# Kernel tuning notes

Hardware: AMD Instinct MI355X
Metric: run time of the kernel (lower is better)

Reference implementation:

```python
import jax, jax.numpy as jnp
import numpy as np

B, S, SC, E, H = 2, 2048, 2048, 1024, 16
D = E // H
EPS = 1e-6


def _layernorm(x, g, b):
    m = jnp.mean(x, axis=-1, keepdims=True)
    v = jnp.mean((x - m) ** 2, axis=-1, keepdims=True)
    return (x - m) / jnp.sqrt(v + EPS) * g + b


def _mha(xk, xv, xq, Wk, Wv, Wq, Wo, bo, masked):
    # per-head projections, vectorized over the head axis: [B,Sx,E] x [H,E,D] -> [B,H,Sx,D]
    K = jnp.einsum('bse,hed->bhsd', xk, Wk)
    V = jnp.einsum('bse,hed->bhsd', xv, Wv)
    Q = jnp.einsum('bqe,hed->bhqd', xq, Wq)
    scores = jnp.einsum('bhqd,bhkd->bhqk', Q, K)  # [B,H,Sq,Sk]
    sk = xk.shape[1]
    if masked:
        causal = jnp.triu(jnp.ones((xq.shape[1], sk), dtype=bool), k=1)
        scores = jnp.where(causal, -jnp.inf, scores)
    att = jax.nn.softmax(scores / jnp.sqrt(jnp.asarray(sk, scores.dtype)), axis=-1)
    out = jnp.einsum('bhqk,bhkd->bhqd', att, V)
    out = out.transpose(0, 2, 1, 3).reshape(out.shape[0], out.shape[2], -1)  # concat heads -> [B,Sq,E]
    return jax.nn.relu(out @ Wo + bo)  # Dense(emb_sz, relu) output projection


def setup_inputs():
    key = jax.random.key(0)
    ks = jax.random.split(key, 16)
    w = lambda k, shape: jax.random.normal(k, shape, jnp.float32) * 0.02
    return {
        'inputs': jax.random.normal(ks[0], (B, S, E), jnp.float32),
        'context_seq': jax.random.normal(ks[1], (B, SC, E), jnp.float32),
        'Wk1': w(ks[2], (H, E, D)), 'Wv1': w(ks[3], (H, E, D)), 'Wq1': w(ks[4], (H, E, D)),
        'Wo1': w(ks[5], (E, E)), 'bo1': jnp.zeros((E,), jnp.float32),
        'Wk2': w(ks[6], (H, E, D)), 'Wv2': w(ks[7], (H, E, D)), 'Wq2': w(ks[8], (H, E, D)),
        'Wo2': w(ks[9], (E, E)), 'bo2': jnp.zeros((E,), jnp.float32),
        'Wf': w(ks[10], (E, E)), 'bf': jnp.zeros((E,), jnp.float32),
        'g1': jnp.ones((E,), jnp.float32), 'b1': jnp.zeros((E,), jnp.float32),
        'g2': jnp.ones((E,), jnp.float32), 'b2': jnp.zeros((E,), jnp.float32),
        'g3': jnp.ones((E,), jnp.float32), 'b3': jnp.zeros((E,), jnp.float32),
    }


def reference(inputs, context_seq, Wk1, Wv1, Wq1, Wo1, bo1,
              Wk2, Wv2, Wq2, Wo2, bo2, Wf, bf,
              g1, b1, g2, b2, g3, b3):
    # masked multi-head self-attention + residual + LN1 (dropout is identity at inference)
    a = _mha(inputs, inputs, inputs, Wk1, Wv1, Wq1, Wo1, bo1, masked=True)
    a = _layernorm(inputs + a, g1, b1)
    # unmasked cross-attention: K/V from context, Q from previous output
    c = _mha(context_seq, context_seq, a, Wk2, Wv2, Wq2, Wo2, bo2, masked=False)
    c = _layernorm(c + c, g2, b2)  # faithful to source: residual adds output to itself
    # FFN (single Dense(emb_sz, relu)) + residual + LN3
    f = jax.nn.relu(c @ Wf + bf)
    return _layernorm(c + f, g3, b3)
```

## Files before the change

### kernel.cpp

```cpp
#include <hip/hip_runtime.h>
#include <stdint.h>
#include <stddef.h>

typedef __bf16 bf16;
typedef __bf16 bf16x8 __attribute__((ext_vector_type(8)));
typedef __bf16 bf16x4 __attribute__((ext_vector_type(4)));
typedef float  f32x4  __attribute__((ext_vector_type(4)));
typedef uint32_t u32x4 __attribute__((ext_vector_type(4)));

#define MFMA(a, b, c) __builtin_amdgcn_mfma_f32_16x16x32_bf16((a), (b), (c), 0, 0, 0)
#define SWZE(row, chunk) (((row) << 6) + ((((chunk) ^ ((row) & 7))) << 3))

static __device__ __forceinline__ void gload_lds16(const void* g, void* l) {
  __builtin_amdgcn_global_load_lds((const __attribute__((address_space(1))) void*)g,
                                   (__attribute__((address_space(3))) void*)l,
                                   16, 0, 0);
}
static __device__ __forceinline__ void waitvm0() {
  asm volatile("s_waitcnt vmcnt(0)" ::: "memory");
}
static __device__ __forceinline__ float expq(float x) {
  float r;
  asm("v_exp_f32 %0, %1" : "=v"(r) : "v"(x));
  return r;
}
static __device__ __forceinline__ float rcpq(float x) {
  float r;
  asm("v_rcp_f32 %0, %1" : "=v"(r) : "v"(x));
  return r;
}
static __device__ __forceinline__ uint32_t cvtpk_bf16(float lo, float hi) {
  uint32_t r;
  asm("v_cvt_pk_bf16_f32 %0, %1, %2" : "=v"(r) : "v"(lo), "v"(hi));
  return r;
}
static __device__ __forceinline__ int xcd_swz(int orig, int nwg) {
  return (orig & 7) * (nwg >> 3) + (orig >> 3);
}
static __device__ __forceinline__ int vperm_store(int s) {
  return (s & ~31) | (((s >> 3) & 1) << 4) | (((s >> 2) & 1) << 3) |
         (((s >> 4) & 1) << 2) | (s & 3);
}

__global__ __launch_bounds__(256) void prep_k(
    const float* __restrict__ inp, const float* __restrict__ ctx,
    bf16* __restrict__ XB, bf16* __restrict__ CB,
    const float* __restrict__ Wq1, const float* __restrict__ Wk1,
    const float* __restrict__ Wv1, const float* __restrict__ Wq2,
    const float* __restrict__ Wk2, const float* __restrict__ Wv2,
    bf16* __restrict__ WQKV1, bf16* __restrict__ WQ2, bf16* __restrict__ WKV2,
    const float* __restrict__ Wo1, const float* __restrict__ Wo2,
    const float* __restrict__ Wf,
    bf16* __restrict__ WO1, bf16* __restrict__ WO2, bf16* __restrict__ WFt) {
  const int tid = threadIdx.x;
  int bx = blockIdx.x;
  if (bx < 8192) {
    const float* s = bx < 4096 ? inp : ctx;
    bf16* d = bx < 4096 ? XB : CB;
    size_t idx = (size_t)(bx & 4095) * 256 + tid;
    float4 v = *(const float4*)(s + idx * 4);
    bf16x4 o;
    o[0] = (bf16)v.x; o[1] = (bf16)v.y; o[2] = (bf16)v.z; o[3] = (bf16)v.w;
    *(bf16x4*)(d + idx * 4) = o;
    return;
  }
  bx -= 8192;
  __shared__ float T[64][65];
  if (bx < 1536) {
    const int wi = bx >> 8, sub = bx & 255;
    const float* src = (wi == 0) ? Wq1 : (wi == 1) ? Wk1 : (wi == 2) ? Wv1
                     : (wi == 3) ? Wq2 : (wi == 4) ? Wk2 : Wv2;
    bf16* dst = (wi == 0) ? WQKV1 : (wi == 1) ? WQKV1 + 1048576
              : (wi == 2) ? WQKV1 + 2097152 : (wi == 3) ? WQ2
              : (wi == 4) ? WKV2 : WKV2 + 1048576;
    const int e0 = (sub & 15) * 64, h = sub >> 4;
    const int er = tid >> 4, dof = (tid & 15) * 4;
#pragma unroll
    for (int i = 0; i < 4; ++i) {
      int e = i * 16 + er;
      float4 v = *(const float4*)(src + ((size_t)h * 1024 + e0 + e) * 64 + dof);
      T[e][dof] = v.x; T[e][dof + 1] = v.y; T[e][dof + 2] = v.z; T[e][dof + 3] = v.w;
    }
    __syncthreads();
    const int dr = tid >> 3, eo = (tid & 7) * 8;
#pragma unroll
    for (int i = 0; i < 2; ++i) {
      int d = i * 32 + dr;
      bf16x8 ov;
#pragma unroll
      for (int j = 0; j < 8; ++j) ov[j] = (bf16)T[eo + j][d];
      *(bf16x8*)(dst + ((size_t)h * 64 + d) * 1024 + e0 + eo) = ov;
    }
    return;
  }
  bx -= 1536;
  {
    const int wi = bx >> 8, sub = bx & 255;
    const float* src = (wi == 0) ? Wo1 : (wi == 1) ? Wo2 : Wf;
    bf16* dst = (wi == 0) ? WO1 : (wi == 1) ? WO2 : WFt;
    const int k0 = (sub & 15) * 64, n0 = (sub >> 4) * 64;
    const int kr = tid >> 4, no = (tid & 15) * 4;
#pragma unroll
    for (int i = 0; i < 4; ++i) {
      int k = i * 16 + kr;
      float4 v = *(const float4*)(src + (size_t)(k0 + k) * 1024 + n0 + no);
      T[k][no] = v.x; T[k][no + 1] = v.y; T[k][no + 2] = v.z; T[k][no + 3] = v.w;
    }
    __syncthreads();
    const int nr = tid >> 3, ko = (tid & 7) * 8;
#pragma unroll
    for (int i = 0; i < 2; ++i) {
      int n = i * 32 + nr;
      bf16x8 ov;
#pragma unroll
      for (int j = 0; j < 8; ++j) ov[j] = (bf16)T[ko + j][n];
      *(bf16x8*)(dst + (size_t)(n0 + n) * 1024 + k0 + ko) = ov;
    }
  }
}

template <int EPI>
static __device__ __forceinline__ void gemm_body(
    const bf16* __restrict__ A, const bf16* __restrict__ Bt,
    bf16* __restrict__ Cb, float* __restrict__ Cf,
    const float* __restrict__ bias, const float* __restrict__ resid,
    int N, int K, float mul, int m0, int n0, bf16* As, bf16* Bs,
    bf16* __restrict__ Vt, int colV) {
  const int tid = threadIdx.x;
  const int l = tid & 63, w = tid >> 6;
  const int l15 = l & 15, g4 = l >> 4;
  const int wr = w >> 1, wc = w & 1;
  f32x4 acc[4][4] = {};
  const int crow = tid >> 3, sj = tid & 7;
  for (int k0 = 0; k0 < K; k0 += 64) {
#pragma unroll
    for (int i = 0; i < 4; ++i) {
      int row = i * 32 + crow;
      int je = ((sj ^ (row & 7)) << 3);
      gload_lds16(A + (size_t)(m0 + row) * K + (k0 + je), (char*)As + (i * 256 + tid) * 16);
      gload_lds16(Bt + (size_t)(n0 + row) * K + (k0 + je), (char*)Bs + (i * 256 + tid) * 16);
    }
    __syncthreads();
#pragma unroll
    for (int kk = 0; kk < 2; ++kk) {
      bf16x8 af[4], bfr[4];
#pragma unroll
      for (int x = 0; x < 4; ++x) {
        af[x]  = *(const bf16x8*)&As[SWZE(wr * 64 + x * 16 + l15, kk * 4 + g4)];
        bfr[x] = *(const bf16x8*)&Bs[SWZE(wc * 64 + x * 16 + l15, kk * 4 + g4)];
      }
      __builtin_amdgcn_s_setprio(1);
#pragma unroll
      for (int mf = 0; mf < 4; ++mf)
#pragma unroll
        for (int nf = 0; nf < 4; ++nf)
          acc[mf][nf] = MFMA(af[mf], bfr[nf], acc[mf][nf]);
      __builtin_amdgcn_s_setprio(0);
    }
    __syncthreads();
  }
  if (EPI == 2 && n0 >= colV) {
#pragma unroll
    for (int mf = 0; mf < 4; ++mf)
#pragma unroll
      for (int nf = 0; nf < 4; ++nf) {
        int colrel = n0 + wc * 64 + nf * 16 + l15 - colV;
        int h = colrel >> 6, d = colrel & 63;
        int row = m0 + wr * 64 + mf * 16 + g4 * 4;
        int b = row >> 11, s = row & 2047;
        bf16x4 pv;
#pragma unroll
        for (int r = 0; r < 4; ++r) pv[r] = (bf16)acc[mf][nf][r];
        *(bf16x4*)(Vt + (((size_t)(b * 16 + h) * 64 + d) * 2048 + vperm_store(s))) = pv;
      }
    return;
  }
#pragma unroll
  for (int mf = 0; mf < 4; ++mf)
#pragma unroll
    for (int nf = 0; nf < 4; ++nf)
#pragma unroll
      for (int r = 0; r < 4; ++r) {
        int row = m0 + wr * 64 + mf * 16 + g4 * 4 + r;
        int col = n0 + wc * 64 + nf * 16 + l15;
        size_t idx = (size_t)row * N + col;
        float v = acc[mf][nf][r];
        if (EPI == 1) {
          v = mul * fmaxf(v + bias[col], 0.f);
          if (resid) v += resid[idx];
          Cf[idx] = v;
        } else {
          Cb[idx] = (bf16)v;
        }
      }
}

__global__ __launch_bounds__(256) void gemm_qkv_k(
    const bf16* __restrict__ A, const bf16* __restrict__ Bt,
    bf16* __restrict__ Cb, bf16* __restrict__ Vt, int N, int K, int colV) {
  __shared__ __align__(16) bf16 As[128 * 64];
  __shared__ __align__(16) bf16 Bs[128 * 64];
  int swz = xcd_swz(blockIdx.y * gridDim.x + blockIdx.x, gridDim.x * gridDim.y);
  int bx = swz % gridDim.x, by = swz / gridDim.x;
  gemm_body<2>(A, Bt, Cb, nullptr, nullptr, nullptr, N, K, 1.f,
               by * 128, bx * 128, As, Bs, Vt, colV);
}

__global__ __launch_bounds__(256) void gemm_bt2_k(
    const bf16* __restrict__ A0, const bf16* __restrict__ Bt0, bf16* __restrict__ C0,
    const bf16* __restrict__ A1, const bf16* __restrict__ Bt1, bf16* __restrict__ C1,
    bf16* __restrict__ Vt, int K) {
  __shared__ __align__(16) bf16 As[128 * 64];
  __shared__ __align__(16) bf16 Bs[128 * 64];
  int swz = xcd_swz(blockIdx.y * gridDim.x + blockIdx.x, gridDim.x * gridDim.y);
  int bx = swz % gridDim.x, by = swz / gridDim.x;
  if (bx < 8)
    gemm_body<0>(A0, Bt0, C0, nullptr, nullptr, nullptr, 1024, K, 1.f,
                 by * 128, bx * 128, As, Bs, nullptr, 1 << 30);
  else
    gemm_body<2>(A1, Bt1, C1, nullptr, nullptr, nullptr, 2048, K, 1.f,
                 by * 128, (bx - 8) * 128, As, Bs, Vt, 1024);
}

template <int EPI>
__global__ __launch_bounds__(512) void gemm64_k(
    const bf16* __restrict__ A, const bf16* __restrict__ Bt,
    bf16* __restrict__ Cb, float* __restrict__ Cf,
    const float* __restrict__ bias, const float* __restrict__ resid,
    int N, int K, float mul) {
  __shared__ __align__(16) bf16 As[64 * 64];
  __shared__ __align__(16) bf16 Bs[128 * 64];
  const int tid = threadIdx.x;
  const int l = tid & 63, w = tid >> 6;
  const int l15 = l & 15, g4 = l >> 4;
  const int wr = w >> 2, wc = w & 3;
  int swz = xcd_swz(blockIdx.y * gridDim.x + blockIdx.x, gridDim.x * gridDim.y);
  const int m0 = (swz / gridDim.x) * 64, n0 = (swz % gridDim.x) * 128;
  f32x4 acc[2][2] = {};
  const int crow = tid >> 3, sj = tid & 7;
  const int jeA = ((sj ^ (crow & 7)) << 3);
  for (int k0 = 0; k0 < K; k0 += 64) {
    gload_lds16(A + (size_t)(m0 + crow) * K + (k0 + jeA), (char*)As + tid * 16);
#pragma unroll
    for (int i = 0; i < 2; ++i) {
      int row = i * 64 + crow;
      int je = ((sj ^ (row & 7)) << 3);
      gload_lds16(Bt + (size_t)(n0 + row) * K + (k0 + je), (char*)Bs + (i * 512 + tid) * 16);
    }
    __syncthreads();
#pragma unroll
    for (int kk = 0; kk < 2; ++kk) {
      bf16x8 af[2], bfr[2];
#pragma unroll
      for (int x = 0; x < 2; ++x) {
        af[x]  = *(const bf16x8*)&As[SWZE(wr * 32 + x * 16 + l15, kk * 4 + g4)];
        bfr[x] = *(const bf16x8*)&Bs[SWZE(wc * 32 + x * 16 + l15, kk * 4 + g4)];
      }
      __builtin_amdgcn_s_setprio(1);
#pragma unroll
      for (int mf = 0; mf < 2; ++mf)
#pragma unroll
        for (int nf = 0; nf < 2; ++nf)
          acc[mf][nf] = MFMA(af[mf], bfr[nf], acc[mf][nf]);
      __builtin_amdgcn_s_setprio(0);
    }
    __syncthreads();
  }
#pragma unroll
  for (int mf = 0; mf < 2; ++mf)
#pragma unroll
    for (int nf = 0; nf < 2; ++nf)
#pragma unroll
      for (int r = 0; r < 4; ++r) {
        int row = m0 + wr * 32 + mf * 16 + g4 * 4 + r;
        int col = n0 + wc * 32 + nf * 16 + l15;
        size_t idx = (size_t)row * N + col;
        float v = acc[mf][nf][r];
        if (EPI == 0) {
          Cb[idx] = (bf16)v;
        } else {
          v = mul * fmaxf(v + bias[col], 0.f);
          if (resid) v += resid[idx];
          Cf[idx] = v;
        }
      }
}

template <int CAUSAL>
__global__ __launch_bounds__(512) void attn_k(
    const bf16* __restrict__ Q, int ldq, size_t sBq,
    const bf16* __restrict__ Kp, int ldk, size_t sBk,
    const bf16* __restrict__ Vt,
    bf16* __restrict__ O, int ldo, size_t sBo,
    int Sk) {
  __shared__ __align__(16) char smem[32768];
  bf16* const KsBase = (bf16*)smem;
  bf16* const VsBase = (bf16*)(smem + 16384);
  const int tid = threadIdx.x;
  const int l = tid & 63, w = tid >> 6;
  const int l15 = l & 15, g4 = l >> 4;
  const int qh = w >> 1, kh = w & 1;
  const int orig = blockIdx.y * gridDim.x + blockIdx.x;
  int qt, bh;
  if (CAUSAL) {
    const int slot = orig >> 8, s = orig & 255;
    const int pb = s & 15;
    qt = slot ? (15 - pb) : pb;
    bh = (s >> 4) * 2 + slot;
  } else {
    const int swz = xcd_swz(orig, gridDim.x * gridDim.y);
    qt = swz % gridDim.x;
    bh = swz / gridDim.x;
  }
  const int b = bh >> 4, h = bh & 15;
  const int nT = Sk >> 6;
  const int total = CAUSAL ? (2 * qt + 2) : nT;
  const int q0b = qt * 128;
  const int qw = q0b + qh * 32;
  const bf16* Qb = Q + (size_t)b * sBq + h * 64;
  const bf16* Kb = Kp + (size_t)b * sBk + h * 64;
  const bf16* Vb = Vt + ((size_t)bh * 64) * Sk;
  bf16* Ob = O + (size_t)b * sBo + h * 64;
  const float sc2 = rsqrtf((float)Sk) * 1.442695040888963f;

  bf16x8 qf[2][2];
#pragma unroll
  for (int qg = 0; qg < 2; ++qg)
#pragma unroll
    for (int kk = 0; kk < 2; ++kk) {
      bf16x8 t8 = *(const bf16x8*)(Qb + (size_t)(qw + qg * 16 + l15) * ldq + kk * 32 + g4 * 8);
#pragma unroll
      for (int j = 0; j < 8; ++j) t8[j] = (bf16)((float)t8[j] * sc2);
      qf[qg][kk] = t8;
    }

  bf16x8 onesb;
#pragma unroll
  for (int j = 0; j < 8; ++j) onesb[j] = (bf16)1.0f;

  f32x4 o[2][4] = {};
  f32x4 ol[2] = {};

  const int srow = tid >> 3, sj = tid & 7;
  const int je = ((sj ^ (srow & 7)) << 3);
  auto stage = [&](int ch, int bufi) {
    gload_lds16(Kb + (size_t)(ch * 64 + srow) * ldk + je,
                (char*)(KsBase + bufi * 4096) + tid * 16);
    gload_lds16(Vb + (size_t)srow * Sk + ch * 64 + je,
                (char*)(VsBase + bufi * 4096) + tid * 16);
  };

  stage(0, 0);
  waitvm0();
  __builtin_amdgcn_s_barrier();

  int cur = 0;

  for (int i = 0; i < total; ++i) {
    if (i + 1 < total) stage(i + 1, cur ^ 1);

    const int k0 = i * 64;
    const bf16* ks = KsBase + cur * 4096;
    const bf16* vs = VsBase + cur * 4096;

    f32x4 s[2][2] = {};
    __builtin_amdgcn_s_setprio(1);
#pragma unroll
    for (int ksub = 0; ksub < 2; ++ksub)
#pragma unroll
      for (int kk = 0; kk < 2; ++kk) {
        bf16x8 kf = *(const bf16x8*)&ks[SWZE(kh * 32 + ksub * 16 + l15, kk * 4 + g4)];
        s[ksub][0] = MFMA(kf, qf[0][kk], s[ksub][0]);
        s[ksub][1] = MFMA(kf, qf[1][kk], s[ksub][1]);
      }
    __builtin_amdgcn_s_setprio(0);

    if (CAUSAL && i >= total - 2) {
#pragma unroll
      for (int ksub = 0; ksub < 2; ++ksub)
#pragma unroll
        for (int qg = 0; qg < 2; ++qg)
#pragma unroll
          for (int r = 0; r < 4; ++r)
            if ((k0 + kh * 32 + ksub * 16 + g4 * 4 + r) > (qw + qg * 16 + l15))
              s[ksub][qg][r] = -3e38f;
    }

#pragma unroll
    for (int ksub = 0; ksub < 2; ++ksub)
#pragma unroll
      for (int qg = 0; qg < 2; ++qg) {
        s[ksub][qg][0] = expq(s[ksub][qg][0]);
        s[ksub][qg][1] = expq(s[ksub][qg][1]);
        s[ksub][qg][2] = expq(s[ksub][qg][2]);
        s[ksub][qg][3] = expq(s[ksub][qg][3]);
      }

    bf16x8 vf[4];
#pragma unroll
    for (int nf2 = 0; nf2 < 4; ++nf2)
      vf[nf2] = *(const bf16x8*)&vs[SWZE(nf2 * 16 + l15, kh * 4 + g4)];

    __builtin_amdgcn_s_setprio(1);
#pragma unroll
    for (int qg = 0; qg < 2; ++qg) {
      u32x4 td;
      td[0] = cvtpk_bf16(s[0][qg][0], s[0][qg][1]);
      td[1] = cvtpk_bf16(s[0][qg][2], s[0][qg][3]);
      td[2] = cvtpk_bf16(s[1][qg][0], s[1][qg][1]);
      td[3] = cvtpk_bf16(s[1][qg][2], s[1][qg][3]);
      bf16x8 pa = __builtin_bit_cast(bf16x8, td);
#pragma unroll
      for (int nf2 = 0; nf2 < 4; ++nf2)
        o[qg][nf2] = MFMA(pa, vf[nf2], o[qg][nf2]);
      ol[qg] = MFMA(pa, onesb, ol[qg]);
    }
    __builtin_amdgcn_s_setprio(0);

    waitvm0();
    __builtin_amdgcn_s_barrier();
    cur ^= 1;
  }

  {
    float* sc = (float*)smem;
    float* my = sc + (size_t)(qh * 64 + l) * 21;
#pragma unroll
    for (int qg = 0; qg < 2; ++qg) {
      __syncthreads();
      if (kh == 1) {
#pragma unroll
        for (int nf2 = 0; nf2 < 4; ++nf2)
#pragma unroll
          for (int r = 0; r < 4; ++r) my[nf2 * 4 + r] = o[qg][nf2][r];
#pragma unroll
        for (int r = 0; r < 4; ++r) my[16 + r] = ol[qg][r];
      }
      __syncthreads();
      if (kh == 0) {
        float inv[4];
#pragma unroll
        for (int r = 0; r < 4; ++r) inv[r] = rcpq(ol[qg][r] + my[16 + r]);
#pragma unroll
        for (int nf2 = 0; nf2 < 4; ++nf2)
#pragma unroll
          for (int r = 0; r < 4; ++r) {
            float v = (o[qg][nf2][r] + my[nf2 * 4 + r]) * inv[r];
            Ob[(size_t)(qw + qg * 16 + g4 * 4 + r) * ldo + nf2 * 16 + l15] = (bf16)v;
          }
      }
    }
  }
}

__global__ __launch_bounds__(256) void ln_k(const float* __restrict__ X,
                                            const float* __restrict__ g,
                                            const float* __restrict__ bta,
                                            bf16* __restrict__ outb,
                                            float* __restrict__ outf) {
  const int tid = threadIdx.x;
  const size_t row = blockIdx.x;
  const float* x = X + row * 1024;
  float4 v = *(const float4*)(x + tid * 4);
  float sum = v.x + v.y + v.z + v.w;
  float sq = v.x * v.x + v.y * v.y + v.z * v.z + v.w * v.w;
#pragma unroll
  for (int m = 1; m < 64; m <<= 1) {
    sum += __shfl_xor(sum, m);
    sq += __shfl_xor(sq, m);
  }
  __shared__ float s1[4], s2[4];
  int w = tid >> 6;
  if ((tid & 63) == 0) { s1[w] = sum; s2[w] = sq; }
  __syncthreads();
  sum = s1[0] + s1[1] + s1[2] + s1[3];
  sq = s2[0] + s2[1] + s2[2] + s2[3];
  float mean = sum * (1.f / 1024.f);
  float var = sq * (1.f / 1024.f) - mean * mean;
  float inv = rsqrtf(var + 1e-6f);
  float4 gv = *(const float4*)(g + tid * 4);
  float4 bv = *(const float4*)(bta + tid * 4);
  float y0 = (v.x - mean) * inv * gv.x + bv.x;
  float y1 = (v.y - mean) * inv * gv.y + bv.y;
  float y2 = (v.z - mean) * inv * gv.z + bv.z;
  float y3 = (v.w - mean) * inv * gv.w + bv.w;
  if (outb) {
    bf16x4 ob;
    ob[0] = (bf16)y0; ob[1] = (bf16)y1; ob[2] = (bf16)y2; ob[3] = (bf16)y3;
    *(bf16x4*)(outb + row * 1024 + tid * 4) = ob;
  }
  if (outf) {
    float4 of;
    of.x = y0; of.y = y1; of.z = y2; of.w = y3;
    *(float4*)(outf + row * 1024 + tid * 4) = of;
  }
}

extern "C" void kernel_launch(void* const* d_in, const int* in_sizes, int n_in,
                              void* d_out, int out_size, void* d_ws, size_t ws_size,
                              hipStream_t stream) {
  (void)in_sizes; (void)n_in; (void)out_size; (void)ws_size;
  const float* inp = (const float*)d_in[0];
  const float* ctx = (const float*)d_in[1];
  const float* Wk1 = (const float*)d_in[2];
  const float* Wv1 = (const float*)d_in[3];
  const float* Wq1 = (const float*)d_in[4];
  const float* Wo1 = (const float*)d_in[5];
  const float* bo1 = (const float*)d_in[6];
  const float* Wk2 = (const float*)d_in[7];
  const float* Wv2 = (const float*)d_in[8];
  const float* Wq2 = (const float*)d_in[9];
  const float* Wo2 = (const float*)d_in[10];
  const float* bo2 = (const float*)d_in[11];
  const float* Wf = (const float*)d_in[12];
  const float* bfp = (const float*)d_in[13];
  const float* g1 = (const float*)d_in[14];
  const float* b1 = (const float*)d_in[15];
  const float* g2 = (const float*)d_in[16];
  const float* b2 = (const float*)d_in[17];
  const float* g3 = (const float*)d_in[18];
  const float* b3 = (const float*)d_in[19];
  float* out = (float*)d_out;

  char* ws = (char*)d_ws;
  size_t off = 0;
  auto alloc = [&](size_t bytes) {
    char* p = ws + off;
    off += (bytes + 255) & ~(size_t)255;
    return p;
  };
  bf16* XB = (bf16*)alloc(4096ULL * 1024 * 2);
  bf16* CB = (bf16*)alloc(4096ULL * 1024 * 2);
  bf16* WQKV1 = (bf16*)alloc(3072ULL * 1024 * 2);
  bf16* WO1 = (bf16*)alloc(1024ULL * 1024 * 2);
  bf16* WQ2 = (bf16*)alloc(1024ULL * 1024 * 2);
  bf16* WKV2 = (bf16*)alloc(2048ULL * 1024 * 2);
  bf16* WO2 = (bf16*)alloc(1024ULL * 1024 * 2);
  bf16* WFt = (bf16*)alloc(1024ULL * 1024 * 2);
  bf16* QKV1 = (bf16*)alloc(4096ULL * 3072 * 2);
  bf16* V1T = (bf16*)alloc(32ULL * 64 * 2048 * 2);
  bf16* ATT1 = (bf16*)alloc(4096ULL * 1024 * 2);
  float* T1 = (float*)alloc(4096ULL * 1024 * 4);
  float* CF = (float*)alloc(4096ULL * 1024 * 4);

  bf16* AB = XB;
  bf16* CBf = CB;
  bf16* Q2 = QKV1;
  bf16* KV2 = QKV1 + 4096ULL * 1024;
  bf16* V2T = V1T;
  bf16* ATT2 = ATT1;
  float* T2 = T1;
  float* T3 = T1;

  dim3 b256(256);
  dim3 b512(512);

  prep_k<<<10496, b256, 0, stream>>>(inp, ctx, XB, CB,
                                     Wq1, Wk1, Wv1, Wq2, Wk2, Wv2,
                                     WQKV1, WQ2, WKV2,
                                     Wo1, Wo2, Wf, WO1, WO2, WFt);

  gemm_qkv_k<<<dim3(24, 32), b256, 0, stream>>>(XB, WQKV1, QKV1, V1T, 3072, 1024, 2048);
  attn_k<1><<<dim3(16, 32), b512, 0, stream>>>(QKV1, 3072, (size_t)2048 * 3072,
                                               QKV1 + 1024, 3072, (size_t)2048 * 3072,
                                               V1T, ATT1, 1024, (size_t)2048 * 1024, 2048);
  gemm64_k<1><<<dim3(8, 64), b512, 0, stream>>>(ATT1, WO1, nullptr, T1, bo1, inp,
                                                1024, 1024, 1.f);
  ln_k<<<4096, b256, 0, stream>>>(T1, g1, b1, AB, nullptr);

  gemm_bt2_k<<<dim3(24, 32), b256, 0, stream>>>(AB, WQ2, Q2, CB, WKV2, KV2, V2T, 1024);
  attn_k<0><<<dim3(16, 32), b512, 0, stream>>>(Q2, 1024, (size_t)2048 * 1024,
                                               KV2, 2048, (size_t)2048 * 2048,
                                               V2T, ATT2, 1024, (size_t)2048 * 1024, 2048);
  gemm64_k<1><<<dim3(8, 64), b512, 0, stream>>>(ATT2, WO2, nullptr, T2, bo2, nullptr,
                                                1024, 1024, 2.f);
  ln_k<<<4096, b256, 0, stream>>>(T2, g2, b2, CBf, CF);

  gemm64_k<1><<<dim3(8, 64), b512, 0, stream>>>(CBf, WFt, nullptr, T3, bfp, CF,
                                                1024, 1024, 1.f);
  ln_k<<<4096, b256, 0, stream>>>(T3, g3, b3, nullptr, out);
}
```

Baseline: 218.3 us.

## Split causal attention KV range across two blocks and add combine kernel

The causal self-attention kernel now splits each query tile's key range into two halves, each handled by a separate block, doubling the grid to 1024 blocks. Each block writes unnormalized partial outputs (bf16) and row sums to scratch buffers, and a new combine kernel adds the halves and normalizes into the attention output. This replaces the previous load-balancing pairing of short and long query tiles with an even split of work per block. It adds a second launch and extra global traffic for the partials, and it rounds the partial sums to bf16 before combining.

```diff
diff --git a/kernel.cpp b/kernel.cpp
--- a/kernel.cpp
+++ b/kernel.cpp
@@ -286,13 +286,13 @@
       }
 }
 
-template <int CAUSAL>
+template <int MODE>
 __global__ __launch_bounds__(512) void attn_k(
     const bf16* __restrict__ Q, int ldq, size_t sBq,
     const bf16* __restrict__ Kp, int ldk, size_t sBk,
     const bf16* __restrict__ Vt,
     bf16* __restrict__ O, int ldo, size_t sBo,
-    int Sk) {
+    int Sk, bf16* __restrict__ Opart, float* __restrict__ Lpart) {
   __shared__ __align__(16) char smem[32768];
   bf16* const KsBase = (bf16*)smem;
   bf16* const VsBase = (bf16*)(smem + 16384);
@@ -301,12 +301,10 @@
   const int l15 = l & 15, g4 = l >> 4;
   const int qh = w >> 1, kh = w & 1;
   const int orig = blockIdx.y * gridDim.x + blockIdx.x;
-  int qt, bh;
-  if (CAUSAL) {
-    const int slot = orig >> 8, s = orig & 255;
-    const int pb = s & 15;
-    qt = slot ? (15 - pb) : pb;
-    bh = (s >> 4) * 2 + slot;
+  int qt, bh, half = 0, rest = 0;
+  if (MODE == 1) {
+    half = orig >> 9; rest = orig & 511;
+    bh = rest >> 4; qt = rest & 15;
   } else {
     const int swz = xcd_swz(orig, gridDim.x * gridDim.y);
     qt = swz % gridDim.x;
@@ -314,7 +312,8 @@
   }
   const int b = bh >> 4, h = bh & 15;
   const int nT = Sk >> 6;
-  const int total = CAUSAL ? (2 * qt + 2) : nT;
+  const int nCh = (MODE == 1) ? (qt + 1) : nT;
+  const int chStart = (MODE == 1) ? half * (qt + 1) : 0;
   const int q0b = qt * 128;
   const int qw = q0b + qh * 32;
   const bf16* Qb = Q + (size_t)b * sBq + h * 64;
@@ -350,16 +349,17 @@
                 (char*)(VsBase + bufi * 4096) + tid * 16);
   };
 
-  stage(0, 0);
+  stage(chStart, 0);
   waitvm0();
   __builtin_amdgcn_s_barrier();
 
   int cur = 0;
 
-  for (int i = 0; i < total; ++i) {
-    if (i + 1 < total) stage(i + 1, cur ^ 1);
-
-    const int k0 = i * 64;
+  for (int i = 0; i < nCh; ++i) {
+    if (i + 1 < nCh) stage(chStart + i + 1, cur ^ 1);
+
+    const int gch = chStart + i;
+    const int k0 = gch * 64;
     const bf16* ks = KsBase + cur * 4096;
     const bf16* vs = VsBase + cur * 4096;
 
@@ -375,7 +375,8 @@
       }
     __builtin_amdgcn_s_setprio(0);
 
-    if (CAUSAL && i >= total - 2) {
+    bool needMask = (MODE == 1) ? (gch >= 2 * qt) : false;
+    if (needMask) {
 #pragma unroll
       for (int ksub = 0; ksub < 2; ++ksub)
 #pragma unroll
@@ -438,18 +439,59 @@
       }
       __syncthreads();
       if (kh == 0) {
-        float inv[4];
-#pragma unroll
-        for (int r = 0; r < 4; ++r) inv[r] = rcpq(ol[qg][r] + my[16 + r]);
-#pragma unroll
-        for (int nf2 = 0; nf2 < 4; ++nf2)
-#pragma unroll
-          for (int r = 0; r < 4; ++r) {
-            float v = (o[qg][nf2][r] + my[nf2 * 4 + r]) * inv[r];
-            Ob[(size_t)(qw + qg * 16 + g4 * 4 + r) * ldo + nf2 * 16 + l15] = (bf16)v;
+        if (MODE == 1) {
+          bf16* op = Opart + (size_t)orig * 8192;
+          float* lp = Lpart + (size_t)orig * 128;
+#pragma unroll
+          for (int nf2 = 0; nf2 < 4; ++nf2)
+#pragma unroll
+            for (int r = 0; r < 4; ++r) {
+              float v = o[qg][nf2][r] + my[nf2 * 4 + r];
+              op[(qh * 32 + qg * 16 + g4 * 4 + r) * 64 + nf2 * 16 + l15] = (bf16)v;
+            }
+          if (l15 == 0) {
+#pragma unroll
+            for (int r = 0; r < 4; ++r)
+              lp[qh * 32 + qg * 16 + g4 * 4 + r] = ol[qg][r] + my[16 + r];
           }
-      }
-    }
+        } else {
+          float inv[4];
+#pragma unroll
+          for (int r = 0; r < 4; ++r) inv[r] = rcpq(ol[qg][r] + my[16 + r]);
+#pragma unroll
+          for (int nf2 = 0; nf2 < 4; ++nf2)
+#pragma unroll
+            for (int r = 0; r < 4; ++r) {
+              float v = (o[qg][nf2][r] + my[nf2 * 4 + r]) * inv[r];
+              Ob[(size_t)(qw + qg * 16 + g4 * 4 + r) * ldo + nf2 * 16 + l15] = (bf16)v;
+            }
+        }
+      }
+    }
+  }
+}
+
+__global__ __launch_bounds__(256) void combine_k(
+    const bf16* __restrict__ Opart, const float* __restrict__ Lpart,
+    bf16* __restrict__ ATT) {
+  const int c = blockIdx.x;
+  const int qt = c & 15, bh = c >> 4, b = bh >> 4, h = bh & 15;
+  const bf16* o0 = Opart + (size_t)c * 8192;
+  const bf16* o1 = Opart + (size_t)(512 + c) * 8192;
+  const float* l0 = Lpart + (size_t)c * 128;
+  const float* l1 = Lpart + (size_t)(512 + c) * 128;
+  const int t = threadIdx.x;
+#pragma unroll
+  for (int e = 0; e < 8; ++e) {
+    int idx = e * 1024 + t * 4;
+    int q = idx >> 6, d = idx & 63;
+    float inv = rcpq(l0[q] + l1[q]);
+    bf16x4 a = *(const bf16x4*)(o0 + idx);
+    bf16x4 bb = *(const bf16x4*)(o1 + idx);
+    bf16x4 r;
+#pragma unroll
+    for (int j = 0; j < 4; ++j) r[j] = (bf16)(((float)a[j] + (float)bb[j]) * inv);
+    *(bf16x4*)(ATT + ((size_t)(b * 2048 + qt * 128 + q) * 1024) + h * 64 + d) = r;
   }
 }
 
@@ -542,6 +584,8 @@
   bf16* ATT1 = (bf16*)alloc(4096ULL * 1024 * 2);
   float* T1 = (float*)alloc(4096ULL * 1024 * 4);
   float* CF = (float*)alloc(4096ULL * 1024 * 4);
+  bf16* OPart = (bf16*)alloc(1024ULL * 8192 * 2);
+  float* LPart = (float*)alloc(1024ULL * 128 * 4);
 
   bf16* AB = XB;
   bf16* CBf = CB;
@@ -561,9 +605,11 @@
                                      Wo1, Wo2, Wf, WO1, WO2, WFt);
 
   gemm_qkv_k<<<dim3(24, 32), b256, 0, stream>>>(XB, WQKV1, QKV1, V1T, 3072, 1024, 2048);
-  attn_k<1><<<dim3(16, 32), b512, 0, stream>>>(QKV1, 3072, (size_t)2048 * 3072,
+  attn_k<1><<<dim3(32, 32), b512, 0, stream>>>(QKV1, 3072, (size_t)2048 * 3072,
                                                QKV1 + 1024, 3072, (size_t)2048 * 3072,
-                                               V1T, ATT1, 1024, (size_t)2048 * 1024, 2048);
+                                               V1T, ATT1, 1024, (size_t)2048 * 1024, 2048,
+                                               OPart, LPart);
+  combine_k<<<512, b256, 0, stream>>>(OPart, LPart, ATT1);
   gemm64_k<1><<<dim3(8, 64), b512, 0, stream>>>(ATT1, WO1, nullptr, T1, bo1, inp,
                                                 1024, 1024, 1.f);
   ln_k<<<4096, b256, 0, stream>>>(T1, g1, b1, AB, nullptr);
@@ -571,7 +617,8 @@
   gemm_bt2_k<<<dim3(24, 32), b256, 0, stream>>>(AB, WQ2, Q2, CB, WKV2, KV2, V2T, 1024);
   attn_k<0><<<dim3(16, 32), b512, 0, stream>>>(Q2, 1024, (size_t)2048 * 1024,
                                                KV2, 2048, (size_t)2048 * 2048,
-                                               V2T, ATT2, 1024, (size_t)2048 * 1024, 2048);
+                                               V2T, ATT2, 1024, (size_t)2048 * 1024, 2048,
+                                               nullptr, nullptr);
   gemm64_k<1><<<dim3(8, 64), b512, 0, stream>>>(ATT2, WO2, nullptr, T2, bo2, nullptr,
                                                 1024, 1024, 2.f);
   ln_k<<<4096, b256, 0, stream>>>(T2, g2, b2, CBf, CF);
```

After: 233.5 us. 6.9% more time.
